# Optimization experiments

Measured on AMD Instinct MI355X. Metric: run time of the kernel, lower is better.

## Reference

```python
import jax, jax.numpy as jnp
import numpy as np

B, T, N, FIN, FOUT, EDIM = 2, 32, 64, 64, 64, 16
EPS = 1e-5

def _xavier(key, fan_in, fan_out):
    limit = np.sqrt(6.0 / (fan_in + fan_out))
    return jax.random.uniform(key, (fan_in, fan_out), minval=-limit, maxval=limit, dtype=jnp.float32)

def setup_inputs() -> dict:
    key = jax.random.key(0)
    ks = jax.random.split(key, 8)
    x = jax.random.normal(ks[0], (B, T, N, FIN), dtype=jnp.float32)
    adj = jax.random.uniform(ks[1], (B, N, N), dtype=jnp.float32)
    # edge_net: Linear(1->EDIM), GELU, Linear(EDIM->FIN*FOUT); stored as (in,out)
    ew1 = _xavier(ks[2], 1, EDIM)
    eb1 = jnp.zeros((EDIM,), jnp.float32)
    ew2 = _xavier(ks[3], EDIM, FIN * FOUT)
    eb2 = jnp.zeros((FIN * FOUT,), jnp.float32)
    # node_lin: Linear(FIN->FOUT)
    nw = _xavier(ks[4], FIN, FOUT)
    nb = jnp.zeros((FOUT,), jnp.float32)
    # GraphNorm params (pre_norm -> num_features = FIN)
    gw = jnp.ones((FIN,), jnp.float32)
    gb = jnp.zeros((FIN,), jnp.float32)
    gms = jnp.ones((1,), jnp.float32)
    return {"x": x, "adj": adj, "ew1": ew1, "eb1": eb1, "ew2": ew2, "eb2": eb2,
            "nw": nw, "nb": nb, "gw": gw, "gb": gb, "gms": gms}

def reference(x, adj, ew1, eb1, ew2, eb2, nw, nb, gw, gb, gms):
    # GraphNorm over node axis (dim=-2), pre-norm
    mean = jnp.mean(x, axis=-2, keepdims=True)
    var = jnp.var(x, axis=-2, keepdims=True)  # unbiased=False
    xn = (x - mean * gms) / jnp.sqrt(var + EPS)
    xn = xn * gw + gb  # (B,T,N,FIN)
    # edge-conditioned weights: scalar adj -> (B,N,N,FIN,FOUT)
    ef = adj[..., None]  # (B,N,N,1)
    h = jax.nn.gelu(ef @ ew1 + eb1, approximate=False)  # (B,N,N,EDIM)
    edge_w = (h @ ew2 + eb2).reshape(adj.shape[0], N, N, FIN, FOUT)
    # agg[b,t,i,o] = sum_j sum_f xn[b,t,j,f] * edge_w[b,i,j,f,o]
    agg = jnp.einsum('btjf,bijfo->btio', xn, edge_w)
    y = xn @ nw + nb + agg
    y = jax.nn.gelu(y, approximate=False)  # torch nn.GELU default = exact erf
    return y
```

## Files before the change

### kernel.cpp

```cpp
#include <hip/hip_runtime.h>


#define LSTR 72
#define XSTR 68
#define CE 4

typedef unsigned short u16;
typedef _Float16 f16;
typedef _Float16 f16x8 __attribute__((ext_vector_type(8)));
typedef _Float16 f16x4 __attribute__((ext_vector_type(4)));
typedef float f32x4 __attribute__((ext_vector_type(4)));

__device__ __forceinline__ float bf2f(u16 u) {
    union { unsigned int i; float f; } c; c.i = ((unsigned int)u) << 16; return c.f;
}
__device__ __forceinline__ u16 f2bf(float f) {
    union { float f; unsigned int i; } c; c.f = f;
    unsigned int r = c.i + 0x7FFFu + ((c.i >> 16) & 1u);
    return (u16)(r >> 16);
}
__device__ __forceinline__ float gelu_exact(float v) {
    return 0.5f * v * (1.0f + erff(v * 0.70710678118654752440f));
}
__device__ __forceinline__ float loadf(const void* p, int i, bool bf) {
    return bf ? bf2f(((const u16*)p)[i]) : ((const float*)p)[i];
}
__device__ __forceinline__ int detect_bf16(const void* xp) {
    const u16* u = (const u16*)xp;
    int sane = 0;
    for (int k = 0; k < 64; ++k) {
        int e = (u[k * 2] >> 7) & 0xFF;
        sane += (e >= 100 && e <= 150);
    }
    return sane >= 40;
}

__global__ __launch_bounds__(256) void precomp(
    const void* __restrict__ adj, const void* __restrict__ ew1, const void* __restrict__ eb1,
    const void* __restrict__ ew2, const void* __restrict__ nw, const void* __restrict__ x,
    f16* __restrict__ H, f16* __restrict__ W2t, f16* __restrict__ NWt)
{
    __shared__ int s_bf;
    if (threadIdx.x == 0) s_bf = detect_bf16(x);
    __syncthreads();
    const bool bf = (s_bf != 0);

    int idx = blockIdx.x * 256 + threadIdx.x;
    if (idx < 131072) {
        int b = idx >> 16, rem = idx & 65535, e = rem >> 12, ij = rem & 4095;
        float a = loadf(adj, (b << 12) + ij, bf);
        float v = a * loadf(ew1, e, bf) + loadf(eb1, e, bf);
        H[idx] = (f16)gelu_exact(v);
    } else if (idx < 196608) {
        int k = idx - 131072, e = k >> 12, of = k & 4095, o = of >> 6, f = of & 63;
        W2t[k] = (f16)loadf(ew2, (e << 12) + (f << 6) + o, bf);
    } else if (idx < 200704) {
        int k = idx - 196608, o = k >> 6, f = k & 63;
        NWt[k] = (f16)loadf(nw, (f << 6) + o, bf);
    }
}

__global__ __launch_bounds__(256) void fused_main(
    const void* __restrict__ x, const void* __restrict__ eb2, const void* __restrict__ nb,
    const void* __restrict__ gw, const void* __restrict__ gb, const void* __restrict__ gms,
    const f16* __restrict__ H, const f16* __restrict__ W2t, const f16* __restrict__ NWt,
    void* __restrict__ out)
{
    __shared__ float xraw[64 * XSTR];
    __shared__ f16 xn_lds[64 * LSTR];
    __shared__ f16 zt_lds[CE * 32 * LSTR];
    __shared__ float red1[256];
    __shared__ float red2[256];
    __shared__ float af[64], cf[64], Sv[64], t2o[64];
    __shared__ int s_bf;

    const int tid  = threadIdx.x;
    const int blk  = blockIdx.x;
    const int bt   = blk >> 1;
    const int half = blk & 1;
    const int b    = bt >> 5;
    const int lane = tid & 63;
    const int wave = tid >> 6;
    const int ln   = lane & 15;
    const int q    = lane >> 4;
    const int row  = tid >> 2;
    const int colb = (tid & 3) << 4;

    if (tid == 0) s_bf = detect_bf16(x);
    __syncthreads();
    const bool bf = (s_bf != 0);

    {
        int base = (bt << 12) + (row << 6) + colb;
        if (bf) {
            const uint4* src = (const uint4*)((const u16*)x + base);
            uint4 v0 = src[0], v1 = src[1];
            const u16* p0 = (const u16*)&v0;
            const u16* p1 = (const u16*)&v1;
            #pragma unroll
            for (int k = 0; k < 8; ++k) {
                xraw[row * XSTR + colb + k]     = bf2f(p0[k]);
                xraw[row * XSTR + colb + 8 + k] = bf2f(p1[k]);
            }
        } else {
            const float4* src = (const float4*)((const float*)x + base);
            #pragma unroll
            for (int k = 0; k < 4; ++k) {
                float4 v = src[k];
                xraw[row * XSTR + colb + 4 * k]     = v.x;
                xraw[row * XSTR + colb + 4 * k + 1] = v.y;
                xraw[row * XSTR + colb + 4 * k + 2] = v.z;
                xraw[row * XSTR + colb + 4 * k + 3] = v.w;
            }
        }
    }
    __syncthreads();
    {
        int f = tid & 63, part = tid >> 6;
        float s1 = 0.f, s2 = 0.f;
        #pragma unroll
        for (int r = 0; r < 16; ++r) {
            float v = xraw[(part * 16 + r) * XSTR + f];
            s1 += v; s2 += v * v;
        }
        red1[part * 64 + f] = s1; red2[part * 64 + f] = s2;
    }
    __syncthreads();
    if (tid < 64) {
        float s1 = red1[tid] + red1[64 + tid] + red1[128 + tid] + red1[192 + tid];
        float s2 = red2[tid] + red2[64 + tid] + red2[128 + tid] + red2[192 + tid];
        float mean = s1 * 0.015625f;
        float var  = s2 * 0.015625f - mean * mean;
        float inv  = rsqrtf(var + 1e-5f);
        float gwf = loadf(gw, tid, bf), gbf = loadf(gb, tid, bf), g = loadf(gms, 0, bf);
        float a = inv * gwf;
        af[tid] = a;
        cf[tid] = gbf - mean * g * a;
        Sv[tid] = 64.f * (mean * (1.f - g) * a + gbf);
    }
    __syncthreads();
    {
        #pragma unroll
        for (int k = 0; k < 16; ++k) {
            int col = colb + k;
            xn_lds[row * LSTR + col] = (f16)(xraw[row * XSTR + col] * af[col] + cf[col]);
        }
    }
    {
        int o = tid & 63, part = tid >> 6;
        float s = 0.f;
        #pragma unroll
        for (int r = 0; r < 16; ++r) {
            int f = part * 16 + r;
            s += Sv[f] * loadf(eb2, (f << 6) + o, bf);
        }
        red1[part * 64 + o] = s;
    }
    __syncthreads();
    if (tid < 64)
        t2o[tid] = red1[tid] + red1[64 + tid] + red1[128 + tid] + red1[192 + tid]
                 + loadf(nb, tid, bf);
    __syncthreads();

    f16x8 xa0 = *(const f16x8*)&xn_lds[(wave * 16 + ln) * LSTR + q * 8];
    f16x8 xa1 = *(const f16x8*)&xn_lds[(wave * 16 + ln) * LSTR + 32 + q * 8];

    f32x4 accA[2], accB[2];
    #pragma unroll
    for (int i2 = 0; i2 < 2; ++i2) {
        accA[i2] = (f32x4){0.f, 0.f, 0.f, 0.f};
        accB[i2] = (f32x4){0.f, 0.f, 0.f, 0.f};
    }

    for (int ec = 0; ec < 16 / CE; ++ec) {
        __syncthreads();
        #pragma unroll
        for (int el = 0; el < CE; ++el) {
            int e = ec * CE + el;
            const f16* w2b = W2t + (((e << 6) + (half << 5)) << 6);
            #pragma unroll
            for (int tn = 0; tn < 2; ++tn) {
                const f16* wrow = w2b + ((tn * 16 + ln) << 6);
                f16x8 b0 = *(const f16x8*)(wrow + q * 8);
                f16x8 b1 = *(const f16x8*)(wrow + 32 + q * 8);
                f32x4 z = {0.f, 0.f, 0.f, 0.f};
                z = __builtin_amdgcn_mfma_f32_16x16x32_f16(xa0, b0, z, 0, 0, 0);
                z = __builtin_amdgcn_mfma_f32_16x16x32_f16(xa1, b1, z, 0, 0, 0);
                f16x4 p;
                #pragma unroll
                for (int r = 0; r < 4; ++r) p[r] = (f16)z[r];
                *(f16x4*)&zt_lds[(el * 32 + tn * 16 + ln) * LSTR + wave * 16 + q * 4] = p;
            }
        }
        __syncthreads();
        #pragma unroll
        for (int el = 0; el < CE; ++el) {
            int e = ec * CE + el;
            const f16* hrow = H + (((b * 16 + e) << 12)) + ((wave * 16 + ln) << 6);
            f16x8 ha0 = *(const f16x8*)(hrow + q * 8);
            f16x8 ha1 = *(const f16x8*)(hrow + 32 + q * 8);
            #pragma unroll
            for (int tn = 0; tn < 2; ++tn) {
                f16x8 zb0 = *(const f16x8*)&zt_lds[(el * 32 + tn * 16 + ln) * LSTR + q * 8];
                f16x8 zb1 = *(const f16x8*)&zt_lds[(el * 32 + tn * 16 + ln) * LSTR + 32 + q * 8];
                accA[tn] = __builtin_amdgcn_mfma_f32_16x16x32_f16(ha0, zb0, accA[tn], 0, 0, 0);
                accB[tn] = __builtin_amdgcn_mfma_f32_16x16x32_f16(ha1, zb1, accB[tn], 0, 0, 0);
            }
        }
    }
    #pragma unroll
    for (int tn = 0; tn < 2; ++tn) {
        const f16* nrow = NWt + (((half * 32 + tn * 16 + ln)) << 6);
        f16x8 b0 = *(const f16x8*)(nrow + q * 8);
        f16x8 b1 = *(const f16x8*)(nrow + 32 + q * 8);
        accA[tn] = __builtin_amdgcn_mfma_f32_16x16x32_f16(xa0, b0, accA[tn], 0, 0, 0);
        accB[tn] = __builtin_amdgcn_mfma_f32_16x16x32_f16(xa1, b1, accB[tn], 0, 0, 0);
    }
    {
        if (bf) {
            u16* ob = (u16*)out + (bt << 12);
            #pragma unroll
            for (int tn = 0; tn < 2; ++tn) {
                int o = half * 32 + tn * 16 + ln;
                float add = t2o[o];
                #pragma unroll
                for (int r = 0; r < 4; ++r) {
                    int i = wave * 16 + q * 4 + r;
                    ob[(i << 6) + o] = f2bf(gelu_exact(accA[tn][r] + accB[tn][r] + add));
                }
            }
        } else {
            float* ob = (float*)out + (bt << 12);
            #pragma unroll
            for (int tn = 0; tn < 2; ++tn) {
                int o = half * 32 + tn * 16 + ln;
                float add = t2o[o];
                #pragma unroll
                for (int r = 0; r < 4; ++r) {
                    int i = wave * 16 + q * 4 + r;
                    ob[(i << 6) + o] = gelu_exact(accA[tn][r] + accB[tn][r] + add);
                }
            }
        }
    }
}

extern "C" void kernel_launch(void* const* d_in, const int* in_sizes, int n_in,
                              void* d_out, int out_size, void* d_ws, size_t ws_size,
                              hipStream_t stream) {
    const void* x   = d_in[0];
    const void* adj = d_in[1];
    const void* ew1 = d_in[2];
    const void* eb1 = d_in[3];
    const void* ew2 = d_in[4];
    const void* eb2 = d_in[5];
    const void* nw  = d_in[6];
    const void* nb  = d_in[7];
    const void* gw  = d_in[8];
    const void* gb  = d_in[9];
    const void* gms = d_in[10];

    f16* H   = (f16*)d_ws;
    f16* W2t = H + 131072;
    f16* NWt = W2t + 65536;

    precomp<<<784, 256, 0, stream>>>(adj, ew1, eb1, ew2, nw, x, H, W2t, NWt);
    fused_main<<<128, 256, 0, stream>>>(x, eb2, nb, gw, gb, gms, H, W2t, NWt, d_out);
}
```

Baseline: 93.44 us.

## Fuse precompute kernel into main kernel, computing GELU edge features on the fly

Removes the separate precompute launch. Each block now loads the ew2 and nw weights, transposed to fp16, directly into shared memory. The edge hidden activations H are recomputed in registers from adj using a polynomial GELU for small inputs, with an exact erf fallback for larger ones. This avoids one kernel launch and the workspace round trip. In exchange, every block redundantly recomputes the GELU and reloads the weights from global memory, and shared memory use grows, which may lower occupancy.

```diff
diff --git a/kernel.cpp b/kernel.cpp
--- a/kernel.cpp
+++ b/kernel.cpp
@@ -21,6 +21,18 @@
 }
 __device__ __forceinline__ float gelu_exact(float v) {
     return 0.5f * v * (1.0f + erff(v * 0.70710678118654752440f));
+}
+__device__ __forceinline__ f16 gelu_small(float v) {
+    float g;
+    if (__builtin_expect(fabsf(v) <= 1.0f, 1)) {
+        float z2 = 0.5f * v * v;
+        float p = 1.0f + z2 * (-0.33333333333333f
+                + z2 * (0.1f + z2 * (-0.02380952380952f + z2 * 0.00462962962963f)));
+        g = 0.5f * v * (1.0f + 0.79788456080287f * v * p);
+    } else {
+        g = gelu_exact(v);
+    }
+    return (f16)g;
 }
 __device__ __forceinline__ float loadf(const void* p, int i, bool bf) {
     return bf ? bf2f(((const u16*)p)[i]) : ((const float*)p)[i];
@@ -35,43 +47,22 @@
     return sane >= 40;
 }
 
-__global__ __launch_bounds__(256) void precomp(
-    const void* __restrict__ adj, const void* __restrict__ ew1, const void* __restrict__ eb1,
-    const void* __restrict__ ew2, const void* __restrict__ nw, const void* __restrict__ x,
-    f16* __restrict__ H, f16* __restrict__ W2t, f16* __restrict__ NWt)
-{
-    __shared__ int s_bf;
-    if (threadIdx.x == 0) s_bf = detect_bf16(x);
-    __syncthreads();
-    const bool bf = (s_bf != 0);
-
-    int idx = blockIdx.x * 256 + threadIdx.x;
-    if (idx < 131072) {
-        int b = idx >> 16, rem = idx & 65535, e = rem >> 12, ij = rem & 4095;
-        float a = loadf(adj, (b << 12) + ij, bf);
-        float v = a * loadf(ew1, e, bf) + loadf(eb1, e, bf);
-        H[idx] = (f16)gelu_exact(v);
-    } else if (idx < 196608) {
-        int k = idx - 131072, e = k >> 12, of = k & 4095, o = of >> 6, f = of & 63;
-        W2t[k] = (f16)loadf(ew2, (e << 12) + (f << 6) + o, bf);
-    } else if (idx < 200704) {
-        int k = idx - 196608, o = k >> 6, f = k & 63;
-        NWt[k] = (f16)loadf(nw, (f << 6) + o, bf);
-    }
-}
-
-__global__ __launch_bounds__(256) void fused_main(
-    const void* __restrict__ x, const void* __restrict__ eb2, const void* __restrict__ nb,
-    const void* __restrict__ gw, const void* __restrict__ gb, const void* __restrict__ gms,
-    const f16* __restrict__ H, const f16* __restrict__ W2t, const f16* __restrict__ NWt,
-    void* __restrict__ out)
+__global__ __launch_bounds__(256) void fused_all(
+    const void* __restrict__ x, const void* __restrict__ adj,
+    const void* __restrict__ ew1, const void* __restrict__ eb1,
+    const void* __restrict__ ew2, const void* __restrict__ eb2,
+    const void* __restrict__ nw, const void* __restrict__ nb,
+    const void* __restrict__ gw, const void* __restrict__ gb,
+    const void* __restrict__ gms, void* __restrict__ out)
 {
     __shared__ float xraw[64 * XSTR];
     __shared__ f16 xn_lds[64 * LSTR];
     __shared__ f16 zt_lds[CE * 32 * LSTR];
+    __shared__ f16 w2s[(16 * 32 + 32) * LSTR];
     __shared__ float red1[256];
     __shared__ float red2[256];
     __shared__ float af[64], cf[64], Sv[64], t2o[64];
+    __shared__ float ew1s[16], eb1s[16];
     __shared__ int s_bf;
 
     const int tid  = threadIdx.x;
@@ -89,6 +80,27 @@
     if (tid == 0) s_bf = detect_bf16(x);
     __syncthreads();
     const bool bf = (s_bf != 0);
+    if (tid < 16) { ew1s[tid] = loadf(ew1, tid, bf); eb1s[tid] = loadf(eb1, tid, bf); }
+
+    float adjv[16];
+    {
+        int basea = (b << 12) + ((wave * 16 + ln) << 6);
+        if (bf) {
+            const u16* ap = (const u16*)adj + basea;
+            #pragma unroll
+            for (int k = 0; k < 8; ++k) {
+                adjv[k]     = bf2f(ap[q * 8 + k]);
+                adjv[8 + k] = bf2f(ap[32 + q * 8 + k]);
+            }
+        } else {
+            const float* ap = (const float*)adj + basea;
+            #pragma unroll
+            for (int k = 0; k < 8; ++k) {
+                adjv[k]     = ap[q * 8 + k];
+                adjv[8 + k] = ap[32 + q * 8 + k];
+            }
+        }
+    }
 
     {
         int base = (bt << 12) + (row << 6) + colb;
@@ -147,6 +159,22 @@
         }
     }
     {
+        int olc = tid & 31, fg = tid >> 5;
+        #pragma unroll 4
+        for (int e = 0; e < 16; ++e) {
+            f16x8 tmp;
+            #pragma unroll
+            for (int k = 0; k < 8; ++k)
+                tmp[k] = (f16)loadf(ew2, (e << 12) + ((fg * 8 + k) << 6) + (half << 5) + olc, bf);
+            *(f16x8*)&w2s[(e * 32 + olc) * LSTR + fg * 8] = tmp;
+        }
+        f16x8 tmp;
+        #pragma unroll
+        for (int k = 0; k < 8; ++k)
+            tmp[k] = (f16)loadf(nw, ((fg * 8 + k) << 6) + (half << 5) + olc, bf);
+        *(f16x8*)&w2s[(512 + olc) * LSTR + fg * 8] = tmp;
+    }
+    {
         int o = tid & 63, part = tid >> 6;
         float s = 0.f;
         #pragma unroll
@@ -174,13 +202,13 @@
 
     for (int ec = 0; ec < 16 / CE; ++ec) {
         __syncthreads();
+        f16x8 ha0c[CE], ha1c[CE];
         #pragma unroll
         for (int el = 0; el < CE; ++el) {
             int e = ec * CE + el;
-            const f16* w2b = W2t + (((e << 6) + (half << 5)) << 6);
-            #pragma unroll
-            for (int tn = 0; tn < 2; ++tn) {
-                const f16* wrow = w2b + ((tn * 16 + ln) << 6);
+            #pragma unroll
+            for (int tn = 0; tn < 2; ++tn) {
+                const f16* wrow = &w2s[(e * 32 + tn * 16 + ln) * LSTR];
                 f16x8 b0 = *(const f16x8*)(wrow + q * 8);
                 f16x8 b1 = *(const f16x8*)(wrow + 32 + q * 8);
                 f32x4 z = {0.f, 0.f, 0.f, 0.f};
@@ -191,26 +219,28 @@
                 for (int r = 0; r < 4; ++r) p[r] = (f16)z[r];
                 *(f16x4*)&zt_lds[(el * 32 + tn * 16 + ln) * LSTR + wave * 16 + q * 4] = p;
             }
+            float w1 = ew1s[e], b1e = eb1s[e];
+            #pragma unroll
+            for (int k = 0; k < 8; ++k) {
+                ha0c[el][k] = gelu_small(adjv[k] * w1 + b1e);
+                ha1c[el][k] = gelu_small(adjv[8 + k] * w1 + b1e);
+            }
         }
         __syncthreads();
         #pragma unroll
         for (int el = 0; el < CE; ++el) {
-            int e = ec * CE + el;
-            const f16* hrow = H + (((b * 16 + e) << 12)) + ((wave * 16 + ln) << 6);
-            f16x8 ha0 = *(const f16x8*)(hrow + q * 8);
-            f16x8 ha1 = *(const f16x8*)(hrow + 32 + q * 8);
             #pragma unroll
             for (int tn = 0; tn < 2; ++tn) {
                 f16x8 zb0 = *(const f16x8*)&zt_lds[(el * 32 + tn * 16 + ln) * LSTR + q * 8];
                 f16x8 zb1 = *(const f16x8*)&zt_lds[(el * 32 + tn * 16 + ln) * LSTR + 32 + q * 8];
-                accA[tn] = __builtin_amdgcn_mfma_f32_16x16x32_f16(ha0, zb0, accA[tn], 0, 0, 0);
-                accB[tn] = __builtin_amdgcn_mfma_f32_16x16x32_f16(ha1, zb1, accB[tn], 0, 0, 0);
+                accA[tn] = __builtin_amdgcn_mfma_f32_16x16x32_f16(ha0c[el], zb0, accA[tn], 0, 0, 0);
+                accB[tn] = __builtin_amdgcn_mfma_f32_16x16x32_f16(ha1c[el], zb1, accB[tn], 0, 0, 0);
             }
         }
     }
     #pragma unroll
     for (int tn = 0; tn < 2; ++tn) {
-        const f16* nrow = NWt + (((half * 32 + tn * 16 + ln)) << 6);
+        const f16* nrow = &w2s[(512 + tn * 16 + ln) * LSTR];
         f16x8 b0 = *(const f16x8*)(nrow + q * 8);
         f16x8 b1 = *(const f16x8*)(nrow + 32 + q * 8);
         accA[tn] = __builtin_amdgcn_mfma_f32_16x16x32_f16(xa0, b0, accA[tn], 0, 0, 0);
@@ -259,11 +289,8 @@
     const void* gw  = d_in[8];
     const void* gb  = d_in[9];
     const void* gms = d_in[10];
-
-    f16* H   = (f16*)d_ws;
-    f16* W2t = H + 131072;
-    f16* NWt = W2t + 65536;
-
-    precomp<<<784, 256, 0, stream>>>(adj, ew1, eb1, ew2, nw, x, H, W2t, NWt);
-    fused_main<<<128, 256, 0, stream>>>(x, eb2, nb, gw, gb, gms, H, W2t, NWt, d_out);
-}
+    (void)d_ws; (void)ws_size;
+
+    fused_all<<<128, 256, 0, stream>>>(x, adj, ew1, eb1, ew2, eb2, nw, nb,
+                                       gw, gb, gms, d_out);
+}
```

New measurement: 102.4 us. +9.6%, slower.

## Split output features into quarters, stage all edge dims at once, drop syncs

Applied to the files above, without the earlier changes.

The main kernel now splits each (b,t) slice into four output-feature quarters instead of halves, which doubles the grid to 256 blocks. Each block computes all 16 edge-dim Z tiles into a larger LDS buffer in one pass, so the chunked loop and its per-chunk barriers go away, and the reduction uses four independent accumulators. The bf16 detection is now computed per thread instead of via a shared flag and barrier. The costs are a larger LDS footprint, redundant per-thread detection loads, and duplicated normalization work across four blocks per slice.

```diff
diff --git a/kernel.cpp b/kernel.cpp
--- a/kernel.cpp
+++ b/kernel.cpp
@@ -3,7 +3,6 @@
 
 #define LSTR 72
 #define XSTR 68
-#define CE 4
 
 typedef unsigned short u16;
 typedef _Float16 f16;
@@ -28,6 +27,7 @@
 __device__ __forceinline__ int detect_bf16(const void* xp) {
     const u16* u = (const u16*)xp;
     int sane = 0;
+    #pragma unroll
     for (int k = 0; k < 64; ++k) {
         int e = (u[k * 2] >> 7) & 0xFF;
         sane += (e >= 100 && e <= 150);
@@ -40,10 +40,7 @@
     const void* __restrict__ ew2, const void* __restrict__ nw, const void* __restrict__ x,
     f16* __restrict__ H, f16* __restrict__ W2t, f16* __restrict__ NWt)
 {
-    __shared__ int s_bf;
-    if (threadIdx.x == 0) s_bf = detect_bf16(x);
-    __syncthreads();
-    const bool bf = (s_bf != 0);
+    const bool bf = detect_bf16(x) != 0;
 
     int idx = blockIdx.x * 256 + threadIdx.x;
     if (idx < 131072) {
@@ -68,16 +65,15 @@
 {
     __shared__ float xraw[64 * XSTR];
     __shared__ f16 xn_lds[64 * LSTR];
-    __shared__ f16 zt_lds[CE * 32 * LSTR];
+    __shared__ f16 zt_lds[16 * 16 * LSTR];
     __shared__ float red1[256];
     __shared__ float red2[256];
     __shared__ float af[64], cf[64], Sv[64], t2o[64];
-    __shared__ int s_bf;
 
     const int tid  = threadIdx.x;
     const int blk  = blockIdx.x;
-    const int bt   = blk >> 1;
-    const int half = blk & 1;
+    const int bt   = blk >> 2;
+    const int quar = blk & 3;
     const int b    = bt >> 5;
     const int lane = tid & 63;
     const int wave = tid >> 6;
@@ -86,9 +82,7 @@
     const int row  = tid >> 2;
     const int colb = (tid & 3) << 4;
 
-    if (tid == 0) s_bf = detect_bf16(x);
-    __syncthreads();
-    const bool bf = (s_bf != 0);
+    const bool bf = detect_bf16(x) != 0;
 
     {
         int base = (bt << 12) + (row << 6) + colb;
@@ -160,86 +154,65 @@
     if (tid < 64)
         t2o[tid] = red1[tid] + red1[64 + tid] + red1[128 + tid] + red1[192 + tid]
                  + loadf(nb, tid, bf);
-    __syncthreads();
 
     f16x8 xa0 = *(const f16x8*)&xn_lds[(wave * 16 + ln) * LSTR + q * 8];
     f16x8 xa1 = *(const f16x8*)&xn_lds[(wave * 16 + ln) * LSTR + 32 + q * 8];
 
-    f32x4 accA[2], accB[2];
     #pragma unroll
-    for (int i2 = 0; i2 < 2; ++i2) {
-        accA[i2] = (f32x4){0.f, 0.f, 0.f, 0.f};
-        accB[i2] = (f32x4){0.f, 0.f, 0.f, 0.f};
-    }
-
-    for (int ec = 0; ec < 16 / CE; ++ec) {
-        __syncthreads();
-        #pragma unroll
-        for (int el = 0; el < CE; ++el) {
-            int e = ec * CE + el;
-            const f16* w2b = W2t + (((e << 6) + (half << 5)) << 6);
-            #pragma unroll
-            for (int tn = 0; tn < 2; ++tn) {
-                const f16* wrow = w2b + ((tn * 16 + ln) << 6);
-                f16x8 b0 = *(const f16x8*)(wrow + q * 8);
-                f16x8 b1 = *(const f16x8*)(wrow + 32 + q * 8);
-                f32x4 z = {0.f, 0.f, 0.f, 0.f};
-                z = __builtin_amdgcn_mfma_f32_16x16x32_f16(xa0, b0, z, 0, 0, 0);
-                z = __builtin_amdgcn_mfma_f32_16x16x32_f16(xa1, b1, z, 0, 0, 0);
-                f16x4 p;
-                #pragma unroll
-                for (int r = 0; r < 4; ++r) p[r] = (f16)z[r];
-                *(f16x4*)&zt_lds[(el * 32 + tn * 16 + ln) * LSTR + wave * 16 + q * 4] = p;
-            }
-        }
-        __syncthreads();
-        #pragma unroll
-        for (int el = 0; el < CE; ++el) {
-            int e = ec * CE + el;
-            const f16* hrow = H + (((b * 16 + e) << 12)) + ((wave * 16 + ln) << 6);
-            f16x8 ha0 = *(const f16x8*)(hrow + q * 8);
-            f16x8 ha1 = *(const f16x8*)(hrow + 32 + q * 8);
-            #pragma unroll
-            for (int tn = 0; tn < 2; ++tn) {
-                f16x8 zb0 = *(const f16x8*)&zt_lds[(el * 32 + tn * 16 + ln) * LSTR + q * 8];
-                f16x8 zb1 = *(const f16x8*)&zt_lds[(el * 32 + tn * 16 + ln) * LSTR + 32 + q * 8];
-                accA[tn] = __builtin_amdgcn_mfma_f32_16x16x32_f16(ha0, zb0, accA[tn], 0, 0, 0);
-                accB[tn] = __builtin_amdgcn_mfma_f32_16x16x32_f16(ha1, zb1, accB[tn], 0, 0, 0);
-            }
-        }
-    }
+    for (int e = 0; e < 16; ++e) {
+        const f16* wrow = W2t + (((e << 6) + (quar << 4) + ln) << 6);
+        f16x8 b0 = *(const f16x8*)(wrow + q * 8);
+        f16x8 b1 = *(const f16x8*)(wrow + 32 + q * 8);
+        f32x4 z = {0.f, 0.f, 0.f, 0.f};
+        z = __builtin_amdgcn_mfma_f32_16x16x32_f16(xa0, b0, z, 0, 0, 0);
+        z = __builtin_amdgcn_mfma_f32_16x16x32_f16(xa1, b1, z, 0, 0, 0);
+        f16x4 p;
+        #pragma unroll
+        for (int r = 0; r < 4; ++r) p[r] = (f16)z[r];
+        *(f16x4*)&zt_lds[((e << 4) + ln) * LSTR + wave * 16 + q * 4] = p;
+    }
+    __syncthreads();
+
+    f32x4 acc0 = {0.f,0.f,0.f,0.f}, acc1 = {0.f,0.f,0.f,0.f};
+    f32x4 acc2 = {0.f,0.f,0.f,0.f}, acc3 = {0.f,0.f,0.f,0.f};
+    const f16* hbase = H + ((b * 16) << 12) + ((wave * 16 + ln) << 6) + q * 8;
     #pragma unroll
-    for (int tn = 0; tn < 2; ++tn) {
-        const f16* nrow = NWt + (((half * 32 + tn * 16 + ln)) << 6);
+    for (int kk = 0; kk < 32; ++kk) {
+        const int e = kk >> 1, jh = kk & 1;
+        f16x8 ha = *(const f16x8*)(hbase + (e << 12) + jh * 32);
+        f16x8 zb = *(const f16x8*)&zt_lds[((e << 4) + ln) * LSTR + jh * 32 + q * 8];
+        switch (kk & 3) {
+            case 0: acc0 = __builtin_amdgcn_mfma_f32_16x16x32_f16(ha, zb, acc0, 0, 0, 0); break;
+            case 1: acc1 = __builtin_amdgcn_mfma_f32_16x16x32_f16(ha, zb, acc1, 0, 0, 0); break;
+            case 2: acc2 = __builtin_amdgcn_mfma_f32_16x16x32_f16(ha, zb, acc2, 0, 0, 0); break;
+            default: acc3 = __builtin_amdgcn_mfma_f32_16x16x32_f16(ha, zb, acc3, 0, 0, 0); break;
+        }
+    }
+    {
+        const f16* nrow = NWt + (((quar << 4) + ln) << 6);
         f16x8 b0 = *(const f16x8*)(nrow + q * 8);
         f16x8 b1 = *(const f16x8*)(nrow + 32 + q * 8);
-        accA[tn] = __builtin_amdgcn_mfma_f32_16x16x32_f16(xa0, b0, accA[tn], 0, 0, 0);
-        accB[tn] = __builtin_amdgcn_mfma_f32_16x16x32_f16(xa1, b1, accB[tn], 0, 0, 0);
-    }
-    {
+        acc0 = __builtin_amdgcn_mfma_f32_16x16x32_f16(xa0, b0, acc0, 0, 0, 0);
+        acc1 = __builtin_amdgcn_mfma_f32_16x16x32_f16(xa1, b1, acc1, 0, 0, 0);
+    }
+    {
+        const int o = (quar << 4) + ln;
+        const float add = t2o[o];
         if (bf) {
             u16* ob = (u16*)out + (bt << 12);
             #pragma unroll
-            for (int tn = 0; tn < 2; ++tn) {
-                int o = half * 32 + tn * 16 + ln;
-                float add = t2o[o];
-                #pragma unroll
-                for (int r = 0; r < 4; ++r) {
-                    int i = wave * 16 + q * 4 + r;
-                    ob[(i << 6) + o] = f2bf(gelu_exact(accA[tn][r] + accB[tn][r] + add));
-                }
+            for (int r = 0; r < 4; ++r) {
+                int i = wave * 16 + q * 4 + r;
+                float v = acc0[r] + acc1[r] + acc2[r] + acc3[r] + add;
+                ob[(i << 6) + o] = f2bf(gelu_exact(v));
             }
         } else {
             float* ob = (float*)out + (bt << 12);
             #pragma unroll
-            for (int tn = 0; tn < 2; ++tn) {
-                int o = half * 32 + tn * 16 + ln;
-                float add = t2o[o];
-                #pragma unroll
-                for (int r = 0; r < 4; ++r) {
-                    int i = wave * 16 + q * 4 + r;
-                    ob[(i << 6) + o] = gelu_exact(accA[tn][r] + accB[tn][r] + add);
-                }
+            for (int r = 0; r < 4; ++r) {
+                int i = wave * 16 + q * 4 + r;
+                float v = acc0[r] + acc1[r] + acc2[r] + acc3[r] + add;
+                ob[(i << 6) + o] = gelu_exact(v);
             }
         }
     }
@@ -265,5 +238,5 @@
     f16* NWt = W2t + 65536;
 
     precomp<<<784, 256, 0, stream>>>(adj, ew1, eb1, ew2, nw, x, H, W2t, NWt);
-    fused_main<<<128, 256, 0, stream>>>(x, eb2, nb, gw, gb, gms, H, W2t, NWt, d_out);
-}
+    fused_main<<<256, 256, 0, stream>>>(x, eb2, nb, gw, gb, gms, H, W2t, NWt, d_out);
+}
```

After: 91.07 us. -2.5%, faster.
